# Kernel optimization log

Hardware: AMD Instinct MI355X
Metric: run time of the kernel (lower is better)

## Reference

```python
import jax, jax.numpy as jnp
import numpy as np

B, F, T, L = 65536, 512, 8, 4


def setup_inputs() -> dict:
    key = jax.random.key(0)
    k1, k2, k3, k4, k5 = jax.random.split(key, 5)
    scale = 1.0 / np.sqrt(F)  # keep the 4-deep cross stack numerically tame
    return {
        "x": jax.random.normal(k1, (B, F), dtype=jnp.float32),
        "cross_w": jax.random.normal(k2, (L, F), dtype=jnp.float32) * scale,
        "cross_b": jax.random.normal(k3, (L, F), dtype=jnp.float32) * 0.1,
        "W_out": jax.random.normal(k4, (F, T), dtype=jnp.float32) * scale,
        "b_out": jax.random.normal(k5, (T,), dtype=jnp.float32) * 0.1,
    }


def reference(x, cross_w, cross_b, W_out, b_out):
    # DCN cross layers. torch does bmm(x0[:, :, None], x[:, None, :]) -> [B,F,F]
    # then tensordot with weights over the last axis; algebraically identical to
    # x0 * (x . w), which we compute directly (no O(B*F*F) intermediate).
    x0 = x
    for i in range(L):  # small fixed layer loop
        s = jnp.einsum("bf,f->b", x, cross_w[i])  # [B]
        x = x0 * s[:, None] + cross_b[i] + x
    return x @ W_out + b_out  # final Linear [B, T]
```

## Files before the change

### kernel.cpp

```cpp
#include <hip/hip_runtime.h>
#include <hip/hip_bf16.h>


typedef float v4f __attribute__((ext_vector_type(4)));
typedef float f32x4 __attribute__((ext_vector_type(4)));
typedef short s16x8 __attribute__((ext_vector_type(8)));

__device__ __forceinline__ short f2bf(float v) {
  return __builtin_bit_cast(short, __float2bfloat16(v));
}
__device__ __forceinline__ float bf2f(short s) {
  return __uint_as_float(((unsigned)(unsigned short)s) << 16);
}

template<int CTRL>
__device__ __forceinline__ float dpp_add(float v) {
  int t = __builtin_amdgcn_update_dpp(0, __float_as_int(v), CTRL, 0xF, 0xF, true);
  return v + __int_as_float(t);
}
__device__ __forceinline__ float wave_reduce(float v) {
  v = dpp_add<0x111>(v); v = dpp_add<0x112>(v); v = dpp_add<0x114>(v);
  v = dpp_add<0x118>(v); v = dpp_add<0x142>(v); v = dpp_add<0x143>(v);
  return v;
}

__global__ __launch_bounds__(256, 4) void cross_one(
    const float* __restrict__ x, const float* __restrict__ cw,
    const float* __restrict__ cb, const float* __restrict__ Wo,
    const float* __restrict__ bo, float* __restrict__ out)
{
  __shared__ s16x8 Bh[16][64];
  __shared__ float ct[4][16][17];

  const int tid = threadIdx.x, lane = tid & 63, wv = tid >> 6;
  const int row0 = (blockIdx.x << 6) + (wv << 4);
  const float* xr = x + (size_t)(row0 + (lane & 15)) * 512 + ((lane >> 4) << 3);

  v4f xa[6], xb[6];
  #pragma unroll
  for (int p = 0; p < 6; ++p) {
    xa[p] = *(const v4f*)(xr + p * 32);
    xb[p] = *(const v4f*)(xr + p * 32 + 4);
  }

  #pragma unroll
  for (int slot = 0; slot < 4; ++slot) {
    const int s = (tid >> 6) + (slot << 2);
    const int l = tid & 63;
    const int c = l & 15, k0 = s * 32 + ((l >> 4) << 3);
    float f[8];
    if (c < 4) {
      v4f a = *(const v4f*)(cw + c * 512 + k0);
      v4f b = *(const v4f*)(cw + c * 512 + k0 + 4);
      #pragma unroll
      for (int j = 0; j < 4; ++j) { f[j] = a[j]; f[4 + j] = b[j]; }
    } else if (c < 12) {
      #pragma unroll
      for (int j = 0; j < 8; ++j) f[j] = Wo[(k0 + j) * 8 + (c - 4)];
    } else {
      #pragma unroll
      for (int j = 0; j < 8; ++j) f[j] = 0.f;
    }
    s16x8 h;
    #pragma unroll
    for (int j = 0; j < 8; ++j) h[j] = f2bf(f[j]);
    Bh[s][l] = h;
  }
  __syncthreads();

  f32x4 acc = {0.f, 0.f, 0.f, 0.f};
  #pragma unroll
  for (int s = 0; s < 16; ++s) {
    const int cur = s % 6;
    const v4f pa = xa[cur], pb = xb[cur];
    if (s + 6 < 16) {
      xa[cur] = *(const v4f*)(xr + (s + 6) * 32);
      xb[cur] = *(const v4f*)(xr + (s + 6) * 32 + 4);
    }
    const s16x8 bh = Bh[s][lane];
    s16x8 ah, al;
    #pragma unroll
    for (int j = 0; j < 4; ++j) {
      ah[j]     = f2bf(pa[j]); al[j]     = f2bf(pa[j] - bf2f(ah[j]));
      ah[4 + j] = f2bf(pb[j]); al[4 + j] = f2bf(pb[j] - bf2f(ah[4 + j]));
    }
    acc = __builtin_amdgcn_mfma_f32_16x16x32_bf16(ah, bh, acc, 0, 0, 0);
    acc = __builtin_amdgcn_mfma_f32_16x16x32_bf16(al, bh, acc, 0, 0, 0);
  }

  float e1, e2, e3, gg[8];
  {
    const int f0 = lane << 3;
    v4f d0a = *(const v4f*)(cb + f0),        d0b = *(const v4f*)(cb + f0 + 4);
    v4f c1a = *(const v4f*)(cb + 512 + f0),  c1b = *(const v4f*)(cb + 512 + f0 + 4);
    v4f c2a = *(const v4f*)(cb + 1024 + f0), c2b = *(const v4f*)(cb + 1024 + f0 + 4);
    v4f c3a = *(const v4f*)(cb + 1536 + f0), c3b = *(const v4f*)(cb + 1536 + f0 + 4);
    v4f w1a = *(const v4f*)(cw + 512 + f0),  w1b = *(const v4f*)(cw + 512 + f0 + 4);
    v4f w2a = *(const v4f*)(cw + 1024 + f0), w2b = *(const v4f*)(cw + 1024 + f0 + 4);
    v4f w3a = *(const v4f*)(cw + 1536 + f0), w3b = *(const v4f*)(cw + 1536 + f0 + 4);
    float e1p = 0.f, e2p = 0.f, e3p = 0.f;
    v4f dA = d0a, dB = d0b;
    #pragma unroll
    for (int e = 0; e < 4; ++e) e1p += dA[e] * w1a[e] + dB[e] * w1b[e];
    dA += c1a; dB += c1b;
    #pragma unroll
    for (int e = 0; e < 4; ++e) e2p += dA[e] * w2a[e] + dB[e] * w2b[e];
    dA += c2a; dB += c2b;
    #pragma unroll
    for (int e = 0; e < 4; ++e) e3p += dA[e] * w3a[e] + dB[e] * w3b[e];
    dA += c3a; dB += c3b;
    float gp[8] = {0.f,0.f,0.f,0.f,0.f,0.f,0.f,0.f};
    #pragma unroll
    for (int e = 0; e < 4; ++e) {
      const float* wra = Wo + (f0 + e) * 8;
      const float* wrb = Wo + (f0 + 4 + e) * 8;
      #pragma unroll
      for (int t = 0; t < 8; ++t) gp[t] += dA[e] * wra[t] + dB[e] * wrb[t];
    }
    e1p = wave_reduce(e1p); e2p = wave_reduce(e2p); e3p = wave_reduce(e3p);
    #pragma unroll
    for (int t = 0; t < 8; ++t) gp[t] = wave_reduce(gp[t]);
    e1 = __shfl(e1p, 63); e2 = __shfl(e2p, 63); e3 = __shfl(e3p, 63);
    #pragma unroll
    for (int t = 0; t < 8; ++t) gg[t] = __shfl(gp[t], 63) + bo[t];
  }

  #pragma unroll
  for (int j = 0; j < 4; ++j)
    ct[wv][((lane >> 4) << 2) + j][lane & 15] = acc[j];
  __builtin_amdgcn_s_waitcnt(0);
  if (lane < 16) {
    const float u0 = ct[wv][lane][0], u1 = ct[wv][lane][1];
    const float u2 = ct[wv][lane][2], u3 = ct[wv][lane][3];
    const float cc1 = 1.f + u0;
    const float cc2 = fmaf(cc1, u1, cc1) + e1;
    const float cc3 = fmaf(cc2, u2, cc2) + e2;
    const float cc4 = fmaf(cc3, u3, cc3) + e3;
    v4f o0, o1;
    #pragma unroll
    for (int t = 0; t < 4; ++t) {
      o0[t] = fmaf(cc4, ct[wv][lane][4 + t], gg[t]);
      o1[t] = fmaf(cc4, ct[wv][lane][8 + t], gg[4 + t]);
    }
    float* op = out + (size_t)(row0 + lane) * 8;
    *(v4f*)(op)     = o0;
    *(v4f*)(op + 4) = o1;
  }
}

extern "C" void kernel_launch(void* const* d_in, const int* in_sizes, int n_in,
                              void* d_out, int out_size, void* d_ws, size_t ws_size,
                              hipStream_t stream) {
  const float* x  = (const float*)d_in[0];
  const float* cw = (const float*)d_in[1];
  const float* cb = (const float*)d_in[2];
  const float* Wo = (const float*)d_in[3];
  const float* bo = (const float*)d_in[4];
  float* out = (float*)d_out;
  const int B = in_sizes[0] / 512;
  hipLaunchKernelGGL(cross_one, dim3(B >> 6), dim3(256), 0, stream,
                     x, cw, cb, Wo, bo, out);
}
```

Measured before the change: 35.93 us.

## Split K across wave pairs, halve register buffering, compute epilogue constants once

Each block now handles 32 rows, and two waves share each 16-row tile by splitting the 512-wide reduction in half. Their MFMA partial sums are combined through shared memory. The prefetch depth per wave drops from 6 to 3 stages, and launch bounds ask for 8 blocks per CU, so register use falls and more waves can stay in flight to hide global-load latency on this bandwidth-bound kernel. The bias/weight-derived constants (e1..e3, output offsets) are now computed by one wave and shared through LDS instead of by every wave. The cost is extra __syncthreads barriers, twice as many blocks each rebuilding the bf16 B tile, and an LDS read-modify-write reduction step.

```diff
diff --git a/kernel.cpp b/kernel.cpp
--- a/kernel.cpp
+++ b/kernel.cpp
@@ -24,29 +24,32 @@
   return v;
 }
 
-__global__ __launch_bounds__(256, 4) void cross_one(
+__global__ __launch_bounds__(256, 8) void cross_occ(
     const float* __restrict__ x, const float* __restrict__ cw,
     const float* __restrict__ cb, const float* __restrict__ Wo,
     const float* __restrict__ bo, float* __restrict__ out)
 {
   __shared__ s16x8 Bh[16][64];
-  __shared__ float ct[4][16][17];
+  __shared__ float ct[2][16][17];
+  __shared__ float egs[12];
 
   const int tid = threadIdx.x, lane = tid & 63, wv = tid >> 6;
-  const int row0 = (blockIdx.x << 6) + (wv << 4);
-  const float* xr = x + (size_t)(row0 + (lane & 15)) * 512 + ((lane >> 4) << 3);
+  const int tile = wv >> 1;
+  const int kh   = wv & 1;
+  const int row0 = (blockIdx.x << 5) + (tile << 4);
 
-  v4f xa[6], xb[6];
+  const float* xr = x + (size_t)(row0 + (lane & 15)) * 512 + (kh << 8)
+                      + ((lane >> 4) << 3);
+
+  v4f xa[3], xb[3];
   #pragma unroll
-  for (int p = 0; p < 6; ++p) {
+  for (int p = 0; p < 3; ++p) {
     xa[p] = *(const v4f*)(xr + p * 32);
     xb[p] = *(const v4f*)(xr + p * 32 + 4);
   }
 
-  #pragma unroll
-  for (int slot = 0; slot < 4; ++slot) {
-    const int s = (tid >> 6) + (slot << 2);
-    const int l = tid & 63;
+  for (int slot = tid; slot < 1024; slot += 256) {
+    const int s = slot >> 6, l = slot & 63;
     const int c = l & 15, k0 = s * 32 + ((l >> 4) << 3);
     float f[8];
     if (c < 4) {
@@ -66,49 +69,29 @@
     for (int j = 0; j < 8; ++j) h[j] = f2bf(f[j]);
     Bh[s][l] = h;
   }
-  __syncthreads();
 
-  f32x4 acc = {0.f, 0.f, 0.f, 0.f};
-  #pragma unroll
-  for (int s = 0; s < 16; ++s) {
-    const int cur = s % 6;
-    const v4f pa = xa[cur], pb = xb[cur];
-    if (s + 6 < 16) {
-      xa[cur] = *(const v4f*)(xr + (s + 6) * 32);
-      xb[cur] = *(const v4f*)(xr + (s + 6) * 32 + 4);
+  if (wv == 0) {
+    const int f0 = lane << 3;
+    float e1p = 0.f, e2p = 0.f, e3p = 0.f;
+    v4f dA = *(const v4f*)(cb + f0), dB = *(const v4f*)(cb + f0 + 4);
+    {
+      v4f wa = *(const v4f*)(cw + 512 + f0), wb = *(const v4f*)(cw + 512 + f0 + 4);
+      #pragma unroll
+      for (int e = 0; e < 4; ++e) e1p += dA[e] * wa[e] + dB[e] * wb[e];
     }
-    const s16x8 bh = Bh[s][lane];
-    s16x8 ah, al;
-    #pragma unroll
-    for (int j = 0; j < 4; ++j) {
-      ah[j]     = f2bf(pa[j]); al[j]     = f2bf(pa[j] - bf2f(ah[j]));
-      ah[4 + j] = f2bf(pb[j]); al[4 + j] = f2bf(pb[j] - bf2f(ah[4 + j]));
+    dA += *(const v4f*)(cb + 512 + f0); dB += *(const v4f*)(cb + 512 + f0 + 4);
+    {
+      v4f wa = *(const v4f*)(cw + 1024 + f0), wb = *(const v4f*)(cw + 1024 + f0 + 4);
+      #pragma unroll
+      for (int e = 0; e < 4; ++e) e2p += dA[e] * wa[e] + dB[e] * wb[e];
     }
-    acc = __builtin_amdgcn_mfma_f32_16x16x32_bf16(ah, bh, acc, 0, 0, 0);
-    acc = __builtin_amdgcn_mfma_f32_16x16x32_bf16(al, bh, acc, 0, 0, 0);
-  }
-
-  float e1, e2, e3, gg[8];
-  {
-    const int f0 = lane << 3;
-    v4f d0a = *(const v4f*)(cb + f0),        d0b = *(const v4f*)(cb + f0 + 4);
-    v4f c1a = *(const v4f*)(cb + 512 + f0),  c1b = *(const v4f*)(cb + 512 + f0 + 4);
-    v4f c2a = *(const v4f*)(cb + 1024 + f0), c2b = *(const v4f*)(cb + 1024 + f0 + 4);
-    v4f c3a = *(const v4f*)(cb + 1536 + f0), c3b = *(const v4f*)(cb + 1536 + f0 + 4);
-    v4f w1a = *(const v4f*)(cw + 512 + f0),  w1b = *(const v4f*)(cw + 512 + f0 + 4);
-    v4f w2a = *(const v4f*)(cw + 1024 + f0), w2b = *(const v4f*)(cw + 1024 + f0 + 4);
-    v4f w3a = *(const v4f*)(cw + 1536 + f0), w3b = *(const v4f*)(cw + 1536 + f0 + 4);
-    float e1p = 0.f, e2p = 0.f, e3p = 0.f;
-    v4f dA = d0a, dB = d0b;
-    #pragma unroll
-    for (int e = 0; e < 4; ++e) e1p += dA[e] * w1a[e] + dB[e] * w1b[e];
-    dA += c1a; dB += c1b;
-    #pragma unroll
-    for (int e = 0; e < 4; ++e) e2p += dA[e] * w2a[e] + dB[e] * w2b[e];
-    dA += c2a; dB += c2b;
-    #pragma unroll
-    for (int e = 0; e < 4; ++e) e3p += dA[e] * w3a[e] + dB[e] * w3b[e];
-    dA += c3a; dB += c3b;
+    dA += *(const v4f*)(cb + 1024 + f0); dB += *(const v4f*)(cb + 1024 + f0 + 4);
+    {
+      v4f wa = *(const v4f*)(cw + 1536 + f0), wb = *(const v4f*)(cw + 1536 + f0 + 4);
+      #pragma unroll
+      for (int e = 0; e < 4; ++e) e3p += dA[e] * wa[e] + dB[e] * wb[e];
+    }
+    dA += *(const v4f*)(cb + 1536 + f0); dB += *(const v4f*)(cb + 1536 + f0 + 4);
     float gp[8] = {0.f,0.f,0.f,0.f,0.f,0.f,0.f,0.f};
     #pragma unroll
     for (int e = 0; e < 4; ++e) {
@@ -120,18 +103,51 @@
     e1p = wave_reduce(e1p); e2p = wave_reduce(e2p); e3p = wave_reduce(e3p);
     #pragma unroll
     for (int t = 0; t < 8; ++t) gp[t] = wave_reduce(gp[t]);
-    e1 = __shfl(e1p, 63); e2 = __shfl(e2p, 63); e3 = __shfl(e3p, 63);
+    if (lane == 63) {
+      egs[0] = e1p; egs[1] = e2p; egs[2] = e3p;
+      #pragma unroll
+      for (int t = 0; t < 8; ++t) egs[3 + t] = gp[t] + bo[t];
+    }
+  }
+  __syncthreads();
+
+  f32x4 acc = {0.f, 0.f, 0.f, 0.f};
+  #pragma unroll
+  for (int s = 0; s < 8; ++s) {
+    const int cur = s % 3;
+    const v4f pa = xa[cur], pb = xb[cur];
+    if (s + 3 < 8) {
+      xa[cur] = *(const v4f*)(xr + (s + 3) * 32);
+      xb[cur] = *(const v4f*)(xr + (s + 3) * 32 + 4);
+    }
+    const s16x8 bh = Bh[(kh << 3) + s][lane];
+    s16x8 ah, al;
     #pragma unroll
-    for (int t = 0; t < 8; ++t) gg[t] = __shfl(gp[t], 63) + bo[t];
+    for (int j = 0; j < 4; ++j) {
+      ah[j]     = f2bf(pa[j]); al[j]     = f2bf(pa[j] - bf2f(ah[j]));
+      ah[4 + j] = f2bf(pb[j]); al[4 + j] = f2bf(pb[j] - bf2f(ah[4 + j]));
+    }
+    acc = __builtin_amdgcn_mfma_f32_16x16x32_bf16(ah, bh, acc, 0, 0, 0);
+    acc = __builtin_amdgcn_mfma_f32_16x16x32_bf16(al, bh, acc, 0, 0, 0);
   }
 
-  #pragma unroll
-  for (int j = 0; j < 4; ++j)
-    ct[wv][((lane >> 4) << 2) + j][lane & 15] = acc[j];
-  __builtin_amdgcn_s_waitcnt(0);
-  if (lane < 16) {
-    const float u0 = ct[wv][lane][0], u1 = ct[wv][lane][1];
-    const float u2 = ct[wv][lane][2], u3 = ct[wv][lane][3];
+  if (kh == 0) {
+    #pragma unroll
+    for (int j = 0; j < 4; ++j)
+      ct[tile][((lane >> 4) << 2) + j][lane & 15] = acc[j];
+  }
+  __syncthreads();
+  if (kh == 1) {
+    #pragma unroll
+    for (int j = 0; j < 4; ++j)
+      ct[tile][((lane >> 4) << 2) + j][lane & 15] += acc[j];
+  }
+  __syncthreads();
+
+  if (kh == 0 && lane < 16) {
+    const float e1 = egs[0], e2 = egs[1], e3 = egs[2];
+    const float u0 = ct[tile][lane][0], u1 = ct[tile][lane][1];
+    const float u2 = ct[tile][lane][2], u3 = ct[tile][lane][3];
     const float cc1 = 1.f + u0;
     const float cc2 = fmaf(cc1, u1, cc1) + e1;
     const float cc3 = fmaf(cc2, u2, cc2) + e2;
@@ -139,8 +155,8 @@
     v4f o0, o1;
     #pragma unroll
     for (int t = 0; t < 4; ++t) {
-      o0[t] = fmaf(cc4, ct[wv][lane][4 + t], gg[t]);
-      o1[t] = fmaf(cc4, ct[wv][lane][8 + t], gg[4 + t]);
+      o0[t] = fmaf(cc4, ct[tile][lane][4 + t], egs[3 + t]);
+      o1[t] = fmaf(cc4, ct[tile][lane][8 + t], egs[7 + t]);
     }
     float* op = out + (size_t)(row0 + lane) * 8;
     *(v4f*)(op)     = o0;
@@ -158,6 +174,6 @@
   const float* bo = (const float*)d_in[4];
   float* out = (float*)d_out;
   const int B = in_sizes[0] / 512;
-  hipLaunchKernelGGL(cross_one, dim3(B >> 6), dim3(256), 0, stream,
+  hipLaunchKernelGGL(cross_occ, dim3(B >> 5), dim3(256), 0, stream,
                      x, cw, cb, Wo, bo, out);
 }
```

Result: no change. 36.61 us (+1.9%).
